# Kernel optimization log

Measured on AMD Instinct MI355X. Metric: run time of the kernel, lower is better.

## Reference

```python
import jax, jax.numpy as jnp
import numpy as np

N_NODES = 50000
N_EDGES = 800000
C_IN = 128
HEADS = 4
C_HEAD = 32  # c_out // heads = 128 // 4
NEG_SLOPE = 0.2


def setup_inputs() -> dict:
    key = jax.random.key(0)
    k_x, k_e, k_w, k_as, k_ad, k_b = jax.random.split(key, 6)
    x = jax.random.normal(k_x, (N_NODES, C_IN), dtype=jnp.float32)
    edge_index = jax.random.randint(k_e, (2, N_EDGES), 0, N_NODES, dtype=jnp.int64)
    # xavier_uniform_ with gain=1.414 on lin.weight [H*C, C_IN] -> same bound for W [C_IN, H*C]
    bound = 1.414 * np.sqrt(6.0 / (C_IN + HEADS * C_HEAD))
    W = jax.random.uniform(k_w, (C_IN, HEADS * C_HEAD), minval=-bound, maxval=bound, dtype=jnp.float32)
    # glorot init for attention vectors (PyG default)
    ab = np.sqrt(6.0 / (1 + HEADS * C_HEAD))
    att_src = jax.random.uniform(k_as, (HEADS, C_HEAD), minval=-ab, maxval=ab, dtype=jnp.float32)
    att_dst = jax.random.uniform(k_ad, (HEADS, C_HEAD), minval=-ab, maxval=ab, dtype=jnp.float32)
    bias = jnp.zeros((HEADS * C_HEAD,), dtype=jnp.float32)
    return {"x": x, "edge_index": edge_index, "W": W,
            "att_src": att_src, "att_dst": att_dst, "bias": bias}


def reference(x, edge_index, W, att_src, att_dst, bias):
    N = x.shape[0]
    H, C = att_src.shape
    # Linear projection, per-head split: [N, H, C]
    xl = (x @ W).reshape(N, H, C)
    a_src = jnp.einsum('nhc,hc->nh', xl, att_src)  # [N, H]
    a_dst = jnp.einsum('nhc,hc->nh', xl, att_dst)  # [N, H]

    src, dst = edge_index[0], edge_index[1]
    loop = jnp.arange(N, dtype=edge_index.dtype)
    # GATConv(add_self_loops=True): remove existing self loops, then add one per node.
    src_f = jnp.concatenate([src, loop])  # [E+N]
    dst_f = jnp.concatenate([dst, loop])
    drop = jnp.concatenate([src == dst, jnp.zeros((N,), dtype=bool)])

    e = jax.nn.leaky_relu(a_src[src_f] + a_dst[dst_f], NEG_SLOPE)  # [E+N, H]
    e = jnp.where(drop[:, None], -jnp.inf, e)

    # segment softmax over edges sharing a destination (every node has a self loop -> max is finite)
    m = jax.ops.segment_max(e, dst_f, num_segments=N)          # [N, H]
    ex = jnp.exp(e - m[dst_f])                                  # [E+N, H]
    denom = jax.ops.segment_sum(ex, dst_f, num_segments=N)     # [N, H]
    alpha = ex / denom[dst_f]                                   # [E+N, H]

    msg = xl[src_f] * alpha[:, :, None]                         # [E+N, H, C]
    out = jax.ops.segment_sum(msg, dst_f, num_segments=N)      # [N, H, C]
    out = out.reshape(N, H * C) + bias
    return out / jnp.sqrt(jnp.asarray(H, dtype=out.dtype))
```

## Files before the change

### kernel.cpp

```cpp
#include <hip/hip_runtime.h>
#include <math.h>

#define CDIM 128
#define HEADS 4
#define NEG 0.2f

typedef __attribute__((ext_vector_type(8))) short bf16x8;
typedef __attribute__((ext_vector_type(8))) unsigned short u16x8;
typedef __attribute__((ext_vector_type(4))) float f32x4;

static __device__ __forceinline__ unsigned short f2bf(float f) {
    unsigned u = __float_as_uint(f);
    u += 0x7FFFu + ((u >> 16) & 1u);
    return (unsigned short)(u >> 16);
}
static __device__ __forceinline__ float bf2f(unsigned short s) {
    return __uint_as_float((unsigned)s << 16);
}

#define LDS_STRIDE 136

__global__ __launch_bounds__(256) void wt_kernel(const float* __restrict__ W,
                                                 unsigned short* __restrict__ WT) {
    int f = blockIdx.x * 256 + threadIdx.x;
    int k = f >> 5, c4 = (f & 31) * 4;
    float4 v = *(const float4*)(W + (size_t)k * CDIM + c4);
    WT[(size_t)(c4 + 0) * CDIM + k] = f2bf(v.x);
    WT[(size_t)(c4 + 1) * CDIM + k] = f2bf(v.y);
    WT[(size_t)(c4 + 2) * CDIM + k] = f2bf(v.z);
    WT[(size_t)(c4 + 3) * CDIM + k] = f2bf(v.w);
}

__global__ __launch_bounds__(256) void gemm_hist_kernel(const float* __restrict__ x,
                                                        const unsigned short* __restrict__ WT,
                                                        const float* __restrict__ att_src,
                                                        const float* __restrict__ att_dst,
                                                        unsigned short* __restrict__ xlh,
                                                        float* __restrict__ a_src,
                                                        float* __restrict__ a_dst, int N,
                                                        const int* __restrict__ esrc,
                                                        const int* __restrict__ edst,
                                                        int* __restrict__ counts,
                                                        int* __restrict__ rank, int E,
                                                        int gemmBlocks) {
    __shared__ unsigned short As[64 * LDS_STRIDE];

    if (blockIdx.x >= gemmBlocks) {
        int e = (blockIdx.x - gemmBlocks) * 256 + threadIdx.x;
        if (e < E) {
            int s = esrc[e], d = edst[e];
            if (s != d) rank[e] = atomicAdd(&counts[d], 1);
        }
        return;
    }

    const int tid = threadIdx.x;
    const int row0 = blockIdx.x * 64;

#pragma unroll
    for (int i = 0; i < 8; ++i) {
        int f = tid + i * 256;
        int r = f >> 5, k4 = f & 31;
        float4 v = make_float4(0.f, 0.f, 0.f, 0.f);
        int gr = row0 + r;
        if (gr < N) v = *(const float4*)(x + (size_t)gr * CDIM + k4 * 4);
        ushort4 h;
        h.x = f2bf(v.x); h.y = f2bf(v.y); h.z = f2bf(v.z); h.w = f2bf(v.w);
        *(ushort4*)(&As[r * LDS_STRIDE + k4 * 4]) = h;
    }
    __syncthreads();

    const int wave = tid >> 6;
    const int lane = tid & 63;
    const int m    = lane & 15;
    const int quad = lane >> 4;
    const int wrow = wave * 16;

    bf16x8 a[4];
#pragma unroll
    for (int ks = 0; ks < 4; ++ks)
        a[ks] = *(const bf16x8*)(&As[(wrow + m) * LDS_STRIDE + ks * 32 + quad * 8]);

    f32x4 acc[8];
#pragma unroll
    for (int t = 0; t < 8; ++t) {
        f32x4 c = {0.f, 0.f, 0.f, 0.f};
#pragma unroll
        for (int ks = 0; ks < 4; ++ks) {
            bf16x8 b = *(const bf16x8*)(WT + (size_t)(t * 16 + m) * CDIM + ks * 32 + quad * 8);
            c = __builtin_amdgcn_mfma_f32_16x16x32_bf16(a[ks], b, c, 0, 0, 0);
        }
        acc[t] = c;
    }

#pragma unroll
    for (int t = 0; t < 8; ++t) {
#pragma unroll
        for (int reg = 0; reg < 4; ++reg) {
            int row = row0 + wrow + quad * 4 + reg;
            if (row < N) xlh[(size_t)row * CDIM + t * 16 + m] = f2bf(acc[t][reg]);
        }
    }

    float ps[4][4], pd[4][4];
#pragma unroll
    for (int h = 0; h < 4; ++h)
#pragma unroll
        for (int reg = 0; reg < 4; ++reg) { ps[h][reg] = 0.f; pd[h][reg] = 0.f; }
#pragma unroll
    for (int t = 0; t < 8; ++t) {
        int h = t >> 1;
        float vs = att_src[t * 16 + m];
        float vd = att_dst[t * 16 + m];
#pragma unroll
        for (int reg = 0; reg < 4; ++reg) {
            ps[h][reg] += acc[t][reg] * vs;
            pd[h][reg] += acc[t][reg] * vd;
        }
    }
#pragma unroll
    for (int off = 8; off > 0; off >>= 1) {
#pragma unroll
        for (int h = 0; h < 4; ++h)
#pragma unroll
            for (int reg = 0; reg < 4; ++reg) {
                ps[h][reg] += __shfl_down(ps[h][reg], off, 16);
                pd[h][reg] += __shfl_down(pd[h][reg], off, 16);
            }
    }
    if (m == 0) {
#pragma unroll
        for (int reg = 0; reg < 4; ++reg) {
            int row = row0 + wrow + quad * 4 + reg;
            if (row < N) {
#pragma unroll
                for (int h = 0; h < 4; ++h) {
                    a_src[row * 4 + h] = ps[h][reg];
                    a_dst[row * 4 + h] = pd[h][reg];
                }
            }
        }
    }
}

__global__ __launch_bounds__(256) void scan_fused_kernel(const int* __restrict__ counts,
                                                         int* __restrict__ offsets,
                                                         int* __restrict__ cursor, int N) {
    __shared__ int sh[256];
    __shared__ int baseSh;
    int idx = blockIdx.x * 256 + threadIdx.x;
    int t = threadIdx.x;
    int c = (idx < N) ? counts[idx] : 0;
    sh[t] = c;
    __syncthreads();
    for (int off = 1; off < 256; off <<= 1) {
        int v = (t >= off) ? sh[t - off] : 0;
        __syncthreads();
        sh[t] += v;
        __syncthreads();
    }
    if (t == 255) baseSh = atomicAdd(cursor, sh[255]);
    __syncthreads();
    if (idx < N) offsets[idx] = baseSh + sh[t] - c;
}

__global__ __launch_bounds__(256) void scatter_kernel(const int* __restrict__ src,
                                                      const int* __restrict__ dst,
                                                      const int* __restrict__ offsets,
                                                      const int* __restrict__ rank,
                                                      int* __restrict__ bucket, int E) {
    int e = blockIdx.x * 256 + threadIdx.x;
    if (e >= E) return;
    int s = src[e], d = dst[e];
    if (s == d) return;
    bucket[offsets[d] + rank[e]] = s;
}

__global__ __launch_bounds__(256) void gather_kernel(const int* __restrict__ offsets,
                                                     const int* __restrict__ counts,
                                                     const int* __restrict__ bucket,
                                                     const unsigned short* __restrict__ xlh,
                                                     const float* __restrict__ a_src,
                                                     const float* __restrict__ a_dst,
                                                     const float* __restrict__ bias,
                                                     float* __restrict__ out, int N) {
    const int node = blockIdx.x * 16 + (threadIdx.x >> 4);
    const int lane16 = threadIdx.x & 15;
    if (node >= N) return;
    const int c8 = lane16 * 8;
    const int h = lane16 >> 2;

    const float ad = a_dst[node * 4 + h];
    const int beg = offsets[node];
    const int cnt = counts[node];

    float acc[8];
#pragma unroll
    for (int i = 0; i < 8; ++i) acc[i] = 0.f;
    float den = 0.f;

    int j = 0;
    for (; j + 8 <= cnt; j += 8) {
        int s[8];
#pragma unroll
        for (int q = 0; q < 8; ++q) s[q] = bucket[beg + j + q];
        float e[8];
#pragma unroll
        for (int q = 0; q < 8; ++q) e[q] = a_src[s[q] * 4 + h] + ad;
        u16x8 u[8];
#pragma unroll
        for (int q = 0; q < 8; ++q) u[q] = *(const u16x8*)(xlh + (size_t)s[q] * CDIM + c8);
        float w[8];
#pragma unroll
        for (int q = 0; q < 8; ++q) {
            float eq = e[q] > 0.f ? e[q] : NEG * e[q];
            w[q] = __expf(eq);
        }
#pragma unroll
        for (int q = 0; q < 8; ++q) {
#pragma unroll
            for (int i = 0; i < 8; ++i) acc[i] += w[q] * bf2f(u[q][i]);
            den += w[q];
        }
    }
    for (; j < cnt; ++j) {
        int s = bucket[beg + j];
        float e = a_src[s * 4 + h] + ad;
        u16x8 u = *(const u16x8*)(xlh + (size_t)s * CDIM + c8);
        e = e > 0.f ? e : NEG * e;
        float w = __expf(e);
#pragma unroll
        for (int i = 0; i < 8; ++i) acc[i] += w * bf2f(u[i]);
        den += w;
    }
    float es = a_src[node * 4 + h] + ad;
    es = es > 0.f ? es : NEG * es;
    float ws = __expf(es);
    u16x8 u = *(const u16x8*)(xlh + (size_t)node * CDIM + c8);
#pragma unroll
    for (int i = 0; i < 8; ++i) acc[i] += ws * bf2f(u[i]);
    den += ws;

    float inv = 1.0f / den;
    float4 b0 = *(const float4*)(bias + c8);
    float4 b1 = *(const float4*)(bias + c8 + 4);
    float4 o0, o1;
    o0.x = (acc[0] * inv + b0.x) * 0.5f;
    o0.y = (acc[1] * inv + b0.y) * 0.5f;
    o0.z = (acc[2] * inv + b0.z) * 0.5f;
    o0.w = (acc[3] * inv + b0.w) * 0.5f;
    o1.x = (acc[4] * inv + b1.x) * 0.5f;
    o1.y = (acc[5] * inv + b1.y) * 0.5f;
    o1.z = (acc[6] * inv + b1.z) * 0.5f;
    o1.w = (acc[7] * inv + b1.w) * 0.5f;
    *(float4*)(out + (size_t)node * CDIM + c8) = o0;
    *(float4*)(out + (size_t)node * CDIM + c8 + 4) = o1;
}

extern "C" void kernel_launch(void* const* d_in, const int* in_sizes, int n_in,
                              void* d_out, int out_size, void* d_ws, size_t ws_size,
                              hipStream_t stream) {
    const float* x       = (const float*)d_in[0];
    const int*   ei      = (const int*)d_in[1];
    const float* W       = (const float*)d_in[2];
    const float* att_src = (const float*)d_in[3];
    const float* att_dst = (const float*)d_in[4];
    const float* bias    = (const float*)d_in[5];
    float* out = (float*)d_out;

    const int N = in_sizes[0] / CDIM;
    const int E = in_sizes[1] / 2;
    const int nb = (N + 255) / 256;

    char* wsb = (char*)d_ws;
    unsigned short* xlh = (unsigned short*)wsb;         wsb += (size_t)N * CDIM * sizeof(unsigned short);
    unsigned short* WT  = (unsigned short*)wsb;         wsb += (size_t)CDIM * CDIM * sizeof(unsigned short);
    float* a_src = (float*)wsb;                         wsb += (size_t)N * HEADS * sizeof(float);
    float* a_dst = (float*)wsb;                         wsb += (size_t)N * HEADS * sizeof(float);
    int* counts  = (int*)wsb;                           wsb += (size_t)N * sizeof(int);
    int* cursor  = (int*)wsb;                           wsb += sizeof(int);
    int* offsets = (int*)wsb;                           wsb += (size_t)N * sizeof(int);
    int* rank    = (int*)wsb;                           wsb += (size_t)E * sizeof(int);
    int* bucket  = (int*)wsb;                           wsb += (size_t)E * sizeof(int);

    hipMemsetAsync(counts, 0, ((size_t)N + 1) * sizeof(int), stream);

    wt_kernel<<<16, 256, 0, stream>>>(W, WT);
    const int gemmBlocks = (N + 63) / 64;
    const int histBlocks = (E + 255) / 256;
    gemm_hist_kernel<<<gemmBlocks + histBlocks, 256, 0, stream>>>(
        x, WT, att_src, att_dst, xlh, a_src, a_dst, N, ei, ei + E, counts, rank, E, gemmBlocks);
    scan_fused_kernel<<<nb, 256, 0, stream>>>(counts, offsets, cursor, N);
    scatter_kernel<<<(E + 255) / 256, 256, 0, stream>>>(ei, ei + E, offsets, rank, bucket, E);
    gather_kernel<<<(N + 15) / 16, 256, 0, stream>>>(offsets, counts, bucket, xlh, a_src, a_dst, bias, out, N);
}
```

Measured before the change: 180.8 us.

## Partition destination histogram into eight sub-counters and schedule hist blocks first

Splits the per-destination atomic counters into eight partitions chosen by histogram block index, so concurrent atomics on the same destination land on different addresses. The scan kernel sums the partitions, writes the totals, and computes a per-partition base offset used by the scatter kernel. Histogram blocks are also placed before the GEMM blocks in the launch grid. This adds eight times the counter memory, a larger memset, and more scan reads and writes in exchange for less atomic contention.

```diff
diff --git a/kernel.cpp b/kernel.cpp
--- a/kernel.cpp
+++ b/kernel.cpp
@@ -4,6 +4,7 @@
 #define CDIM 128
 #define HEADS 4
 #define NEG 0.2f
+#define NPART 8
 
 typedef __attribute__((ext_vector_type(8))) short bf16x8;
 typedef __attribute__((ext_vector_type(8))) unsigned short u16x8;
@@ -40,22 +41,27 @@
                                                         float* __restrict__ a_dst, int N,
                                                         const int* __restrict__ esrc,
                                                         const int* __restrict__ edst,
-                                                        int* __restrict__ counts,
+                                                        int* __restrict__ cnt8,
                                                         int* __restrict__ rank, int E,
-                                                        int gemmBlocks) {
+                                                        int histBlocks) {
     __shared__ unsigned short As[64 * LDS_STRIDE];
 
-    if (blockIdx.x >= gemmBlocks) {
-        int e = (blockIdx.x - gemmBlocks) * 256 + threadIdx.x;
+    if ((int)blockIdx.x < histBlocks) {
+        int hb = blockIdx.x;
+        int e = hb * 256 + threadIdx.x;
         if (e < E) {
+            int p = hb & (NPART - 1);
             int s = esrc[e], d = edst[e];
-            if (s != d) rank[e] = atomicAdd(&counts[d], 1);
+            if (s != d) {
+                int r = atomicAdd(&cnt8[p * N + d], 1);
+                rank[e] = r | (p << 20);
+            }
         }
         return;
     }
 
     const int tid = threadIdx.x;
-    const int row0 = blockIdx.x * 64;
+    const int row0 = (blockIdx.x - histBlocks) * 64;
 
 #pragma unroll
     for (int i = 0; i < 8; ++i) {
@@ -143,15 +149,23 @@
     }
 }
 
-__global__ __launch_bounds__(256) void scan_fused_kernel(const int* __restrict__ counts,
+__global__ __launch_bounds__(256) void scan_fused_kernel(const int* __restrict__ cnt8,
+                                                         int* __restrict__ counts,
                                                          int* __restrict__ offsets,
+                                                         int* __restrict__ base8,
                                                          int* __restrict__ cursor, int N) {
     __shared__ int sh[256];
     __shared__ int baseSh;
     int idx = blockIdx.x * 256 + threadIdx.x;
     int t = threadIdx.x;
-    int c = (idx < N) ? counts[idx] : 0;
-    sh[t] = c;
+    int c[NPART];
+    int tot = 0;
+#pragma unroll
+    for (int p = 0; p < NPART; ++p) {
+        c[p] = (idx < N) ? cnt8[p * N + idx] : 0;
+        tot += c[p];
+    }
+    sh[t] = tot;
     __syncthreads();
     for (int off = 1; off < 256; off <<= 1) {
         int v = (t >= off) ? sh[t - off] : 0;
@@ -161,19 +175,31 @@
     }
     if (t == 255) baseSh = atomicAdd(cursor, sh[255]);
     __syncthreads();
-    if (idx < N) offsets[idx] = baseSh + sh[t] - c;
+    if (idx < N) {
+        int run = baseSh + sh[t] - tot;
+        counts[idx] = tot;
+        offsets[idx] = run;
+#pragma unroll
+        for (int p = 0; p < NPART; ++p) {
+            base8[p * N + idx] = run;
+            run += c[p];
+        }
+    }
 }
 
 __global__ __launch_bounds__(256) void scatter_kernel(const int* __restrict__ src,
                                                       const int* __restrict__ dst,
-                                                      const int* __restrict__ offsets,
+                                                      const int* __restrict__ base8,
                                                       const int* __restrict__ rank,
-                                                      int* __restrict__ bucket, int E) {
+                                                      int* __restrict__ bucket, int E, int N) {
     int e = blockIdx.x * 256 + threadIdx.x;
     if (e >= E) return;
     int s = src[e], d = dst[e];
     if (s == d) return;
-    bucket[offsets[d] + rank[e]] = s;
+    int rp = rank[e];
+    int p = rp >> 20;
+    int r = rp & 0xFFFFF;
+    bucket[base8[p * N + d] + r] = s;
 }
 
 __global__ __launch_bounds__(256) void gather_kernel(const int* __restrict__ offsets,
@@ -277,20 +303,22 @@
     unsigned short* WT  = (unsigned short*)wsb;         wsb += (size_t)CDIM * CDIM * sizeof(unsigned short);
     float* a_src = (float*)wsb;                         wsb += (size_t)N * HEADS * sizeof(float);
     float* a_dst = (float*)wsb;                         wsb += (size_t)N * HEADS * sizeof(float);
+    int* cnt8    = (int*)wsb;                           wsb += (size_t)NPART * N * sizeof(int);
+    int* cursor  = (int*)wsb;                           wsb += sizeof(int);
     int* counts  = (int*)wsb;                           wsb += (size_t)N * sizeof(int);
-    int* cursor  = (int*)wsb;                           wsb += sizeof(int);
     int* offsets = (int*)wsb;                           wsb += (size_t)N * sizeof(int);
+    int* base8   = (int*)wsb;                           wsb += (size_t)NPART * N * sizeof(int);
     int* rank    = (int*)wsb;                           wsb += (size_t)E * sizeof(int);
     int* bucket  = (int*)wsb;                           wsb += (size_t)E * sizeof(int);
 
-    hipMemsetAsync(counts, 0, ((size_t)N + 1) * sizeof(int), stream);
+    hipMemsetAsync(cnt8, 0, ((size_t)NPART * N + 1) * sizeof(int), stream);
 
     wt_kernel<<<16, 256, 0, stream>>>(W, WT);
+    const int histBlocks = (E + 255) / 256;
     const int gemmBlocks = (N + 63) / 64;
-    const int histBlocks = (E + 255) / 256;
-    gemm_hist_kernel<<<gemmBlocks + histBlocks, 256, 0, stream>>>(
-        x, WT, att_src, att_dst, xlh, a_src, a_dst, N, ei, ei + E, counts, rank, E, gemmBlocks);
-    scan_fused_kernel<<<nb, 256, 0, stream>>>(counts, offsets, cursor, N);
-    scatter_kernel<<<(E + 255) / 256, 256, 0, stream>>>(ei, ei + E, offsets, rank, bucket, E);
+    gemm_hist_kernel<<<histBlocks + gemmBlocks, 256, 0, stream>>>(
+        x, WT, att_src, att_dst, xlh, a_src, a_dst, N, ei, ei + E, cnt8, rank, E, histBlocks);
+    scan_fused_kernel<<<nb, 256, 0, stream>>>(cnt8, counts, offsets, base8, cursor, N);
+    scatter_kernel<<<(E + 255) / 256, 256, 0, stream>>>(ei, ei + E, base8, rank, bucket, E, N);
     gather_kernel<<<(N + 15) / 16, 256, 0, stream>>>(offsets, counts, bucket, xlh, a_src, a_dst, bias, out, N);
 }
```

Measured after the change: 198.6 us. +9.8%, slower.

## Split gather edges across four lane groups and pack dst/rank for scatter

Applied to the files above, without the earlier changes.

The gather kernel now assigns a full 64-lane wavefront per node, splits its incoming edges across four 16-lane groups, and combines partial sums with cross-lane shuffles, to expose more memory parallelism per node. The histogram pass stores destination and rank packed in one 32-bit word, so the scatter reads fewer arrays and processes two edges per thread. The separate memset is folded into the weight-transpose kernel. Packing assumes node ids and per-node ranks fit in 16 bits, which limits generality beyond 65536 nodes.

```diff
diff --git a/kernel.cpp b/kernel.cpp
--- a/kernel.cpp
+++ b/kernel.cpp
@@ -21,8 +21,10 @@
 #define LDS_STRIDE 136
 
 __global__ __launch_bounds__(256) void wt_kernel(const float* __restrict__ W,
-                                                 unsigned short* __restrict__ WT) {
+                                                 unsigned short* __restrict__ WT,
+                                                 int* __restrict__ counts, int nClr) {
     int f = blockIdx.x * 256 + threadIdx.x;
+    for (int i = f; i < nClr; i += 4096) counts[i] = 0;
     int k = f >> 5, c4 = (f & 31) * 4;
     float4 v = *(const float4*)(W + (size_t)k * CDIM + c4);
     WT[(size_t)(c4 + 0) * CDIM + k] = f2bf(v.x);
@@ -41,15 +43,20 @@
                                                         const int* __restrict__ esrc,
                                                         const int* __restrict__ edst,
                                                         int* __restrict__ counts,
-                                                        int* __restrict__ rank, int E,
+                                                        unsigned* __restrict__ packed, int E,
                                                         int gemmBlocks) {
     __shared__ unsigned short As[64 * LDS_STRIDE];
 
-    if (blockIdx.x >= gemmBlocks) {
+    if ((int)blockIdx.x >= gemmBlocks) {
         int e = (blockIdx.x - gemmBlocks) * 256 + threadIdx.x;
         if (e < E) {
             int s = esrc[e], d = edst[e];
-            if (s != d) rank[e] = atomicAdd(&counts[d], 1);
+            unsigned pk = ~0u;
+            if (s != d) {
+                int r = atomicAdd(&counts[d], 1);
+                pk = (unsigned)d | ((unsigned)r << 16);
+            }
+            packed[e] = pk;
         }
         return;
     }
@@ -165,15 +172,23 @@
 }
 
 __global__ __launch_bounds__(256) void scatter_kernel(const int* __restrict__ src,
-                                                      const int* __restrict__ dst,
+                                                      const unsigned* __restrict__ packed,
                                                       const int* __restrict__ offsets,
-                                                      const int* __restrict__ rank,
                                                       int* __restrict__ bucket, int E) {
-    int e = blockIdx.x * 256 + threadIdx.x;
-    if (e >= E) return;
-    int s = src[e], d = dst[e];
-    if (s == d) return;
-    bucket[offsets[d] + rank[e]] = s;
+    int base = (blockIdx.x * 256 + threadIdx.x) * 2;
+    if (base + 2 <= E) {
+        int2 s2 = *(const int2*)(src + base);
+        uint2 p2 = *(const uint2*)(packed + base);
+        int d0 = p2.x & 0xFFFFu, r0 = p2.x >> 16;
+        int d1 = p2.y & 0xFFFFu, r1 = p2.y >> 16;
+        int o0 = offsets[d0];
+        int o1 = offsets[d1];
+        if (p2.x != ~0u) bucket[o0 + r0] = s2.x;
+        if (p2.y != ~0u) bucket[o1 + r1] = s2.y;
+    } else if (base < E) {
+        unsigned pk = packed[base];
+        if (pk != ~0u) bucket[offsets[pk & 0xFFFFu] + (pk >> 16)] = src[base];
+    }
 }
 
 __global__ __launch_bounds__(256) void gather_kernel(const int* __restrict__ offsets,
@@ -184,8 +199,10 @@
                                                      const float* __restrict__ a_dst,
                                                      const float* __restrict__ bias,
                                                      float* __restrict__ out, int N) {
-    const int node = blockIdx.x * 16 + (threadIdx.x >> 4);
-    const int lane16 = threadIdx.x & 15;
+    const int node = blockIdx.x * 4 + (threadIdx.x >> 6);
+    const int lane = threadIdx.x & 63;
+    const int g = lane >> 4;
+    const int lane16 = lane & 15;
     if (node >= N) return;
     const int c8 = lane16 * 8;
     const int h = lane16 >> 2;
@@ -199,31 +216,31 @@
     for (int i = 0; i < 8; ++i) acc[i] = 0.f;
     float den = 0.f;
 
-    int j = 0;
-    for (; j + 8 <= cnt; j += 8) {
-        int s[8];
-#pragma unroll
-        for (int q = 0; q < 8; ++q) s[q] = bucket[beg + j + q];
-        float e[8];
-#pragma unroll
-        for (int q = 0; q < 8; ++q) e[q] = a_src[s[q] * 4 + h] + ad;
-        u16x8 u[8];
-#pragma unroll
-        for (int q = 0; q < 8; ++q) u[q] = *(const u16x8*)(xlh + (size_t)s[q] * CDIM + c8);
-        float w[8];
-#pragma unroll
-        for (int q = 0; q < 8; ++q) {
+    int j = g;
+    for (; j + 12 < cnt; j += 16) {
+        int s[4];
+#pragma unroll
+        for (int q = 0; q < 4; ++q) s[q] = bucket[beg + j + 4 * q];
+        float e[4];
+#pragma unroll
+        for (int q = 0; q < 4; ++q) e[q] = a_src[s[q] * 4 + h] + ad;
+        u16x8 u[4];
+#pragma unroll
+        for (int q = 0; q < 4; ++q) u[q] = *(const u16x8*)(xlh + (size_t)s[q] * CDIM + c8);
+        float w[4];
+#pragma unroll
+        for (int q = 0; q < 4; ++q) {
             float eq = e[q] > 0.f ? e[q] : NEG * e[q];
             w[q] = __expf(eq);
         }
 #pragma unroll
-        for (int q = 0; q < 8; ++q) {
+        for (int q = 0; q < 4; ++q) {
 #pragma unroll
             for (int i = 0; i < 8; ++i) acc[i] += w[q] * bf2f(u[q][i]);
             den += w[q];
         }
     }
-    for (; j < cnt; ++j) {
+    for (; j < cnt; j += 4) {
         int s = bucket[beg + j];
         float e = a_src[s * 4 + h] + ad;
         u16x8 u = *(const u16x8*)(xlh + (size_t)s * CDIM + c8);
@@ -233,28 +250,39 @@
         for (int i = 0; i < 8; ++i) acc[i] += w * bf2f(u[i]);
         den += w;
     }
-    float es = a_src[node * 4 + h] + ad;
-    es = es > 0.f ? es : NEG * es;
-    float ws = __expf(es);
-    u16x8 u = *(const u16x8*)(xlh + (size_t)node * CDIM + c8);
-#pragma unroll
-    for (int i = 0; i < 8; ++i) acc[i] += ws * bf2f(u[i]);
-    den += ws;
-
-    float inv = 1.0f / den;
-    float4 b0 = *(const float4*)(bias + c8);
-    float4 b1 = *(const float4*)(bias + c8 + 4);
-    float4 o0, o1;
-    o0.x = (acc[0] * inv + b0.x) * 0.5f;
-    o0.y = (acc[1] * inv + b0.y) * 0.5f;
-    o0.z = (acc[2] * inv + b0.z) * 0.5f;
-    o0.w = (acc[3] * inv + b0.w) * 0.5f;
-    o1.x = (acc[4] * inv + b1.x) * 0.5f;
-    o1.y = (acc[5] * inv + b1.y) * 0.5f;
-    o1.z = (acc[6] * inv + b1.z) * 0.5f;
-    o1.w = (acc[7] * inv + b1.w) * 0.5f;
-    *(float4*)(out + (size_t)node * CDIM + c8) = o0;
-    *(float4*)(out + (size_t)node * CDIM + c8 + 4) = o1;
+    if (g == 0) {
+        float es = a_src[node * 4 + h] + ad;
+        es = es > 0.f ? es : NEG * es;
+        float ws = __expf(es);
+        u16x8 u = *(const u16x8*)(xlh + (size_t)node * CDIM + c8);
+#pragma unroll
+        for (int i = 0; i < 8; ++i) acc[i] += ws * bf2f(u[i]);
+        den += ws;
+    }
+#pragma unroll
+    for (int i = 0; i < 8; ++i) {
+        acc[i] += __shfl_xor(acc[i], 16);
+        acc[i] += __shfl_xor(acc[i], 32);
+    }
+    den += __shfl_xor(den, 16);
+    den += __shfl_xor(den, 32);
+
+    if (g == 0) {
+        float inv = 1.0f / den;
+        float4 b0 = *(const float4*)(bias + c8);
+        float4 b1 = *(const float4*)(bias + c8 + 4);
+        float4 o0, o1;
+        o0.x = (acc[0] * inv + b0.x) * 0.5f;
+        o0.y = (acc[1] * inv + b0.y) * 0.5f;
+        o0.z = (acc[2] * inv + b0.z) * 0.5f;
+        o0.w = (acc[3] * inv + b0.w) * 0.5f;
+        o1.x = (acc[4] * inv + b1.x) * 0.5f;
+        o1.y = (acc[5] * inv + b1.y) * 0.5f;
+        o1.z = (acc[6] * inv + b1.z) * 0.5f;
+        o1.w = (acc[7] * inv + b1.w) * 0.5f;
+        *(float4*)(out + (size_t)node * CDIM + c8) = o0;
+        *(float4*)(out + (size_t)node * CDIM + c8 + 4) = o1;
+    }
 }
 
 extern "C" void kernel_launch(void* const* d_in, const int* in_sizes, int n_in,
@@ -280,17 +308,15 @@
     int* counts  = (int*)wsb;                           wsb += (size_t)N * sizeof(int);
     int* cursor  = (int*)wsb;                           wsb += sizeof(int);
     int* offsets = (int*)wsb;                           wsb += (size_t)N * sizeof(int);
-    int* rank    = (int*)wsb;                           wsb += (size_t)E * sizeof(int);
+    unsigned* packed = (unsigned*)wsb;                  wsb += (size_t)E * sizeof(unsigned);
     int* bucket  = (int*)wsb;                           wsb += (size_t)E * sizeof(int);
 
-    hipMemsetAsync(counts, 0, ((size_t)N + 1) * sizeof(int), stream);
-
-    wt_kernel<<<16, 256, 0, stream>>>(W, WT);
+    wt_kernel<<<16, 256, 0, stream>>>(W, WT, counts, N + 1);
     const int gemmBlocks = (N + 63) / 64;
     const int histBlocks = (E + 255) / 256;
     gemm_hist_kernel<<<gemmBlocks + histBlocks, 256, 0, stream>>>(
-        x, WT, att_src, att_dst, xlh, a_src, a_dst, N, ei, ei + E, counts, rank, E, gemmBlocks);
+        x, WT, att_src, att_dst, xlh, a_src, a_dst, N, ei, ei + E, counts, packed, E, gemmBlocks);
     scan_fused_kernel<<<nb, 256, 0, stream>>>(counts, offsets, cursor, N);
-    scatter_kernel<<<(E + 255) / 256, 256, 0, stream>>>(ei, ei + E, offsets, rank, bucket, E);
-    gather_kernel<<<(N + 15) / 16, 256, 0, stream>>>(offsets, counts, bucket, xlh, a_src, a_dst, bias, out, N);
-}
+    scatter_kernel<<<((E + 1) / 2 + 255) / 256, 256, 0, stream>>>(ei, packed, offsets, bucket, E);
+    gather_kernel<<<(N + 3) / 4, 256, 0, stream>>>(offsets, counts, bucket, xlh, a_src, a_dst, bias, out, N);
+}
```

After: 180.0 us. About the same (-0.5%).
